# Kernel tuning notes

Measured on AMD Instinct MI355X. Metric: run time of the kernel, lower is better.

Reference implementation:

```python
import jax, jax.numpy as jnp
import numpy as np

NUM_EXPERTS = 4


def _conv1x1(w, b, x):
    # w: [out,in], b: [out], x: [B,in,H,W]
    return jnp.einsum('oc,bchw->bohw', w, x) + b[None, :, None, None]


def _sobel(x):
    c = x.shape[1]
    kx = jnp.array([[-1., 0., 1.], [-2., 0., 2.], [-1., 0., 1.]], dtype=x.dtype)
    ky = jnp.array([[-1., -2., -1.], [0., 0., 0.], [1., 2., 1.]], dtype=x.dtype)
    wx = jnp.broadcast_to(kx[None, None], (c, 1, 3, 3))
    wy = jnp.broadcast_to(ky[None, None], (c, 1, 3, 3))
    dn = ('NCHW', 'OIHW', 'NCHW')
    gx = jax.lax.conv_general_dilated(x, wx, (1, 1), [(1, 1), (1, 1)],
                                      dimension_numbers=dn, feature_group_count=c)
    gy = jax.lax.conv_general_dilated(x, wy, (1, 1), [(1, 1), (1, 1)],
                                      dimension_numbers=dn, feature_group_count=c)
    return gx, gy


def _bilinear_sample(x, gx, gy):
    # torch F.grid_sample(mode='bilinear', padding_mode='zeros', align_corners=False)
    # x: [B,C,H,W]; gx, gy: [B,Hs,Ws] normalized coords in [-1,1]
    B, C, H, W = x.shape
    ix = ((gx + 1.0) * W - 1.0) * 0.5
    iy = ((gy + 1.0) * H - 1.0) * 0.5
    x0 = jnp.floor(ix)
    y0 = jnp.floor(iy)
    wx1 = ix - x0
    wx0 = 1.0 - wx1
    wy1 = iy - y0
    wy0 = 1.0 - wy1
    xf = x.reshape(B, C, H * W)

    def gather(xc, yc):
        valid = (xc >= 0) & (xc <= W - 1) & (yc >= 0) & (yc <= H - 1)
        xi = jnp.clip(xc, 0, W - 1).astype(jnp.int32)
        yi = jnp.clip(yc, 0, H - 1).astype(jnp.int32)
        idx = yi * W + xi  # [B,Hs,Ws]
        v = jax.vmap(lambda xb, ib: xb[:, ib])(xf, idx)  # [B,C,Hs,Ws]
        return v * valid[:, None].astype(x.dtype)

    return (gather(x0, y0) * (wx0 * wy0)[:, None]
            + gather(x0 + 1, y0) * (wx1 * wy0)[:, None]
            + gather(x0, y0 + 1) * (wx0 * wy1)[:, None]
            + gather(x0 + 1, y0 + 1) * (wx1 * wy1)[:, None])


def _forward(x, wc_e, we_e, wb1, bb1, wb2, bb2, wr, br, wo, bo, wcv, bcv, scale, scale2):
    B, c, h, w = x.shape
    sh = round(h * scale)
    sw = round(w * scale2)

    grad_x, grad_y = _sobel(x)

    # relative-offset coordinate embedding, [1,4,sh,sw]
    ih = (jnp.arange(sh, dtype=x.dtype) + 0.5) / scale
    coor_h = ih - jnp.floor(ih + 0.001) - 0.5  # [sh]
    iw = (jnp.arange(sw, dtype=x.dtype) + 0.5) / scale2
    coor_w = iw - jnp.floor(iw + 0.001) - 0.5  # [sw]
    inp = jnp.stack([
        jnp.full((sh, sw), 1.0 / scale2, dtype=x.dtype),
        jnp.full((sh, sw), 1.0 / scale, dtype=x.dtype),
        jnp.broadcast_to(coor_h[:, None], (sh, sw)),
        jnp.broadcast_to(coor_w[None, :], (sh, sw)),
    ], axis=0)[None]

    emb = jax.nn.relu(_conv1x1(wb2, bb2, jax.nn.relu(_conv1x1(wb1, bb1, inp))))
    offset = _conv1x1(wo, bo, emb)                 # [1,2,sh,sw]
    routing = jax.nn.sigmoid(_conv1x1(wr, br, emb))  # [1,E,sh,sw]

    # per-pixel soft mixture of expert compress/expand matrices
    rw = routing.reshape(NUM_EXPERTS, sh * sw).T   # [N,E]
    wc = (rw @ wc_e.reshape(NUM_EXPERTS, -1)).reshape(sh, sw, c // 8, c)
    we = (rw @ we_e.reshape(NUM_EXPERTS, -1)).reshape(sh, sw, c, c // 8)

    feat = _conv1x1(wcv, bcv, jnp.concatenate([x, grad_x, grad_y], axis=1))  # [B,64,h,w]

    # base grid (align_corners=True-style normalization, as in the source) + learned offsets
    gx0 = ((jnp.arange(sw, dtype=x.dtype) + 0.5) / scale2 - 0.5) * 2.0 / (w - 1) - 1.0
    gy0 = ((jnp.arange(sh, dtype=x.dtype) + 0.5) / scale - 0.5) * 2.0 / (h - 1) - 1.0
    gx = jnp.broadcast_to(gx0[None, None, :] + offset[:, 0] * (2.0 / (w - 1)), (B, sh, sw))
    gy = jnp.broadcast_to(gy0[None, :, None] + offset[:, 1] * (2.0 / (h - 1)), (B, sh, sw))

    fea0 = _bilinear_sample(feat, gx, gy)          # [B,64,sh,sw]

    mid = jnp.einsum('hwkc,bchw->bhwk', wc, fea0)  # per-pixel compress (k=C//8)
    out = jnp.einsum('hwck,bhwk->bchw', we, mid)   # per-pixel expand
    return out + fea0


def setup_inputs() -> dict:
    key = jax.random.key(0)
    ks = jax.random.split(key, 13)
    s = 0.05
    return {
        'x': jax.random.normal(ks[0], (2, 64, 192, 192), jnp.float32),
        'weight_compress': jax.random.normal(ks[1], (4, 8, 64), jnp.float32) * s,
        'weight_expand': jax.random.normal(ks[2], (4, 64, 8), jnp.float32) * s,
        'w_body1': jax.random.normal(ks[3], (64, 4), jnp.float32) * s,
        'b_body1': jax.random.normal(ks[4], (64,), jnp.float32) * s,
        'w_body2': jax.random.normal(ks[5], (64, 64), jnp.float32) * s,
        'b_body2': jax.random.normal(ks[6], (64,), jnp.float32) * s,
        'w_routing': jax.random.normal(ks[7], (4, 64), jnp.float32) * s,
        'b_routing': jax.random.normal(ks[8], (4,), jnp.float32) * s,
        'w_offset': jax.random.normal(ks[9], (2, 64), jnp.float32) * s,
        'b_offset': jax.random.normal(ks[10], (2,), jnp.float32) * s,
        'w_conv': jax.random.normal(ks[11], (64, 192), jnp.float32) * s,
        'b_conv': jax.random.normal(ks[12], (64,), jnp.float32) * s,
        'scale': 2,
        'scale2': 2,
    }


def reference(x, weight_compress, weight_expand, w_body1, b_body1, w_body2, b_body2,
              w_routing, b_routing, w_offset, b_offset, w_conv, b_conv, scale, scale2):
    return _forward(x, weight_compress, weight_expand, w_body1, b_body1, w_body2, b_body2,
                    w_routing, b_routing, w_offset, b_offset, w_conv, b_conv, scale, scale2)
```

## Files before the change

### kernel.cpp

```cpp
#include <hip/hip_runtime.h>
#include <hip/hip_bf16.h>
#include <math.h>

#define BN  2
#define CN  64
#define HN  192
#define WN  192
#define SH  384
#define SW  384
#define HW  (HN * WN)
#define NPIX (BN * HN * WN)

typedef __attribute__((ext_vector_type(8))) short bf16x8;
typedef __attribute__((ext_vector_type(4))) float f32x4;

#define CPAD  72
#define TRB   (BN * HN * 3)
#define TBLB  64

__device__ inline unsigned short f2bf(float f) {
    unsigned int u = __float_as_uint(f);
    u += 0x7fffu + ((u >> 16) & 1u);
    return (unsigned short)(u >> 16);
}
__device__ inline unsigned int pkbf(float a, float b) {
    return (unsigned int)f2bf(a) | ((unsigned int)f2bf(b) << 16);
}
__device__ inline float bf2f(unsigned short u) {
    return __uint_as_float((unsigned int)u << 16);
}

__device__ inline void run_mlp(int lane, float in0, float in1, float chv, float cwv,
    const float* __restrict__ wb1, const float* __restrict__ bb1,
    const float* __restrict__ wb2, const float* __restrict__ bb2,
    const float* __restrict__ wr,  const float* __restrict__ wo, float p[6])
{
    float4 w1 = ((const float4*)wb1)[lane];
    float h1 = fmaxf(bb1[lane] + w1.x * in0 + w1.y * in1 + w1.z * chv + w1.w * cwv, 0.f);
    const float4* w2row = (const float4*)(wb2 + lane * 64);
    float acc = bb2[lane];
#pragma unroll
    for (int q = 0; q < 16; ++q) {
        float4 wv = w2row[q];
        acc += wv.x * __shfl(h1, q * 4 + 0)
             + wv.y * __shfl(h1, q * 4 + 1)
             + wv.z * __shfl(h1, q * 4 + 2)
             + wv.w * __shfl(h1, q * 4 + 3);
    }
    float h2 = fmaxf(acc, 0.f);
#pragma unroll
    for (int e = 0; e < 4; ++e) p[e] = wr[e * 64 + lane] * h2;
#pragma unroll
    for (int e = 0; e < 2; ++e) p[4 + e] = wo[e * 64 + lane] * h2;
#pragma unroll
    for (int m = 1; m < 64; m <<= 1) {
#pragma unroll
        for (int e = 0; e < 6; ++e) p[e] += __shfl_xor(p[e], m);
    }
}

__global__ __launch_bounds__(256) void prepass_kernel(
    const float* __restrict__ x,
    const float* __restrict__ wcv,
    const float* __restrict__ wb1, const float* __restrict__ bb1,
    const float* __restrict__ wb2, const float* __restrict__ bb2,
    const float* __restrict__ wr,  const float* __restrict__ br,
    const float* __restrict__ wo,  const float* __restrict__ bo,
    const float* __restrict__ wce, const float* __restrict__ wee,
    const int* __restrict__ scale_p, const int* __restrict__ scale2_p,
    unsigned short* __restrict__ xt,
    unsigned short* __restrict__ tblW,
    float* __restrict__ tblEntry, unsigned short* __restrict__ tblM)
{
    __shared__ __attribute__((aligned(16))) unsigned short sm[64 * CPAD];

    int tid  = threadIdx.x;
    int lane = tid & 63;
    int bi = blockIdx.x;

    if (bi < TRB) {
        int jt = bi % 3;
        int t2 = bi / 3;
        int i  = t2 % HN;
        int b  = t2 / HN;
        int j0 = jt * 64;
        int w  = tid >> 6;
        int c0 = w * 16;

        const float* xp = x + (size_t)b * CN * HW + (size_t)i * WN + j0 + lane;
#pragma unroll
        for (int k = 0; k < 16; k += 2) {
            float f0 = xp[(size_t)(c0 + k) * HW];
            float f1 = xp[(size_t)(c0 + k + 1) * HW];
            *(unsigned int*)(sm + lane * CPAD + c0 + k) = pkbf(f0, f1);
        }
        __syncthreads();
        size_t obase = (((size_t)b * HN + i) * WN + j0) * 64;
#pragma unroll
        for (int it = 0; it < 2; ++it) {
            int task = tid + it * 256;
            int jj = task >> 3, oc = task & 7;
            uint4 v = *(const uint4*)(sm + jj * CPAD + oc * 8);
            *(uint4*)(xt + obase + (size_t)jj * 64 + oc * 8) = v;
        }
        return;
    }

    if (bi == TRB) {
        const float KXc[9] = {-1.f, 0.f, 1.f, -2.f, 0.f, 2.f, -1.f, 0.f, 1.f};
        const float KYc[9] = {-1.f, -2.f, -1.f, 0.f, 0.f, 0.f, 1.f, 2.f, 1.f};
        int wv = tid >> 6;
        int o  = (wv << 4) + (lane & 15);
        const float* wp = wcv + o * 192;
        float v0[2][8], v1[2][8], v2[2][8];
#pragma unroll
        for (int kc = 0; kc < 2; ++kc) {
            int kb = kc * 32 + (lane >> 4) * 8;
            float4 a0 = *(const float4*)(wp + kb);
            float4 a1 = *(const float4*)(wp + kb + 4);
            float4 b0 = *(const float4*)(wp + 64 + kb);
            float4 b1 = *(const float4*)(wp + 64 + kb + 4);
            float4 c0 = *(const float4*)(wp + 128 + kb);
            float4 c1 = *(const float4*)(wp + 128 + kb + 4);
            v0[kc][0]=a0.x; v0[kc][1]=a0.y; v0[kc][2]=a0.z; v0[kc][3]=a0.w;
            v0[kc][4]=a1.x; v0[kc][5]=a1.y; v0[kc][6]=a1.z; v0[kc][7]=a1.w;
            v1[kc][0]=b0.x; v1[kc][1]=b0.y; v1[kc][2]=b0.z; v1[kc][3]=b0.w;
            v1[kc][4]=b1.x; v1[kc][5]=b1.y; v1[kc][6]=b1.z; v1[kc][7]=b1.w;
            v2[kc][0]=c0.x; v2[kc][1]=c0.y; v2[kc][2]=c0.z; v2[kc][3]=c0.w;
            v2[kc][4]=c1.x; v2[kc][5]=c1.y; v2[kc][6]=c1.z; v2[kc][7]=c1.w;
        }
#pragma unroll
        for (int t = 0; t < 9; ++t) {
#pragma unroll
            for (int kc = 0; kc < 2; ++kc) {
                bf16x8 a;
#pragma unroll
                for (int e = 0; e < 8; ++e) {
                    float f = v1[kc][e] * KXc[t] + v2[kc][e] * KYc[t];
                    if (t == 4) f += v0[kc][e];
                    a[e] = (short)f2bf(f);
                }
                *(bf16x8*)(void*)(tblW + (size_t)(((wv * 9 + t) * 2 + kc) * 64 + lane) * 8) = a;
            }
        }
        return;
    }

    {
        float* wcmL = (float*)sm;
        float* wemL = wcmL + 1024;
        float* reL  = wemL + 1024;

        int sc = scale_p[0], sc2 = scale2_p[0];
        float scale = (float)sc, scale2 = (float)sc2;
        float in0 = 1.f / scale2, in1 = 1.f / scale;
        bool fast = (sc2 == 2 && sc <= 16);
        int tb = bi - (TRB + 1);

        if (fast) {
            int pi = tb;
            if (pi >= sc) return;
            if (tid < 64) {
                float ih = (pi + 0.5f) / scale;
                float chv = ih - floorf(ih + 0.001f) - 0.5f;
                float p0[6], p1[6];
                {
                    float iw = 0.5f / scale2;
                    float cwv = iw - floorf(iw + 0.001f) - 0.5f;
                    run_mlp(lane, in0, in1, chv, cwv, wb1, bb1, wb2, bb2, wr, wo, p0);
                }
                {
                    float iw = 1.5f / scale2;
                    float cwv = iw - floorf(iw + 0.001f) - 0.5f;
                    run_mlp(lane, in0, in1, chv, cwv, wb1, bb1, wb2, bb2, wr, wo, p1);
                }
                if (lane == 0) {
                    float* t0 = tblEntry + (pi * 2 + 0) * 8;
                    float* t1 = tblEntry + (pi * 2 + 1) * 8;
#pragma unroll
                    for (int e = 0; e < 4; ++e) {
                        float rE = 1.f / (1.f + expf(-(p0[e] + br[e])));
                        float rO = 1.f / (1.f + expf(-(p1[e] + br[e])));
                        t0[e] = rE; t1[e] = rO;
                        reL[e] = rE; reL[4 + e] = rO;
                    }
                    t0[4] = p0[4] + bo[0]; t0[5] = p0[5] + bo[1];
                    t1[4] = p1[4] + bo[0]; t1[5] = p1[5] + bo[1];
                }
            }
            __syncthreads();
            float reE0 = reL[0], reE1 = reL[1], reE2 = reL[2], reE3 = reL[3];
            float reO0 = reL[4], reO1 = reL[5], reO2 = reL[6], reO3 = reL[7];
            for (int idx = tid; idx < 512; idx += 256) {
                float a = wce[idx], bq = wce[512 + idx], c = wce[1024 + idx], d = wce[1536 + idx];
                wcmL[idx]       = reE0 * a + reE1 * bq + reE2 * c + reE3 * d;
                wcmL[512 + idx] = reO0 * a + reO1 * bq + reO2 * c + reO3 * d;
                float e_ = wee[idx], f = wee[512 + idx], g = wee[1024 + idx], h = wee[1536 + idx];
                wemL[idx]       = reE0 * e_ + reE1 * f + reE2 * g + reE3 * h;
                wemL[512 + idx] = reO0 * e_ + reO1 * f + reO2 * g + reO3 * h;
            }
            __syncthreads();
            int co  = tid >> 2;
            int ci0 = (tid & 3) << 4;
            float w0[8], w1[8];
#pragma unroll
            for (int k = 0; k < 8; ++k) {
                w0[k] = wemL[co * 8 + k];
                w1[k] = wemL[512 + co * 8 + k];
            }
            unsigned short* tbp = tblM + (size_t)pi * 2 * 4096;
#pragma unroll
            for (int cc = 0; cc < 16; ++cc) {
                int ci = ci0 + cc;
                float m0 = 0.f, m1 = 0.f;
#pragma unroll
                for (int k = 0; k < 8; ++k) {
                    m0 += w0[k] * wcmL[k * 64 + ci];
                    m1 += w1[k] * wcmL[512 + k * 64 + ci];
                }
                float avg = 0.5f * (m0 + m1) + ((co == ci) ? 1.f : 0.f);
                tbp[co * 64 + ci]        = f2bf(avg);
                tbp[4096 + co * 64 + ci] = f2bf(0.5f * (m0 - m1));
            }
        } else {
            int w_ = (tb * 256 + tid) >> 6;
            if (w_ >= sc * sc2) return;
            int pi = w_ / sc2, pj = w_ - pi * sc2;
            float ih = (pi + 0.5f) / scale;
            float chv = ih - floorf(ih + 0.001f) - 0.5f;
            float iw = (pj + 0.5f) / scale2;
            float cwv = iw - floorf(iw + 0.001f) - 0.5f;
            float p[6];
            run_mlp(lane, in0, in1, chv, cwv, wb1, bb1, wb2, bb2, wr, wo, p);
            if (lane == 0) {
                float* tp = tblEntry + w_ * 8;
#pragma unroll
                for (int e = 0; e < 4; ++e) tp[e] = 1.f / (1.f + expf(-(p[e] + br[e])));
                tp[4] = p[4] + bo[0];
                tp[5] = p[5] + bo[1];
            }
        }
    }
}

__global__ __launch_bounds__(256) void feat_kernel(
    const unsigned short* __restrict__ xt,
    const unsigned short* __restrict__ tblW,
    const float* __restrict__ bcv,
    unsigned short* __restrict__ featN)
{
    __shared__ __attribute__((aligned(16))) unsigned short sm[198 * CPAD];

    int tid  = threadIdx.x;
    int lane = tid & 63;
    int bi = blockIdx.x;
    int jt = bi % 3;
    int t2 = bi / 3;
    int i0 = t2 % HN;
    int b  = t2 / HN;
    int j0 = jt * 64;
    int w  = __builtin_amdgcn_readfirstlane(tid >> 6);

    int row = lane & 15;
    int q   = lane >> 4;

    bf16x8 afrag[9][2];
#pragma unroll
    for (int t = 0; t < 9; ++t)
#pragma unroll
        for (int kc = 0; kc < 2; ++kc)
            afrag[t][kc] = *(const bf16x8*)(void*)(
                tblW + (size_t)(((w * 9 + t) * 2 + kc) * 64 + lane) * 8);

#pragma unroll
    for (int it = 0; it < 7; ++it) {
        int task = tid + it * 256;
        if (task < 198 * 8) {
            int p  = task >> 3;
            int oc = task & 7;
            int rowi = p / 66;
            int col  = p - rowi * 66;
            int sr = i0 - 1 + rowi;
            int hc = j0 - 1 + col;
            bool ok = (sr >= 0) && (sr < HN) && (hc >= 0) && (hc < WN);
            int srb = ok ? sr : 0;
            int hcb = ok ? hc : 0;
            uint4 v = *(const uint4*)(xt + (((size_t)b * HN + srb) * WN + hcb) * 64 + oc * 8);
            if (!ok) v = (uint4){0u, 0u, 0u, 0u};
            *(uint4*)(sm + p * CPAD + oc * 8) = v;
        }
    }

    __syncthreads();

    f32x4 acc[4] = {};
    const unsigned short* bb0 = sm + row * CPAD + (q << 3);
#pragma unroll
    for (int nt = 0; nt < 4; ++nt) {
#pragma unroll
        for (int t = 0; t < 9; ++t) {
            int a_ = t / 3, dxi = t - a_ * 3;
#pragma unroll
            for (int kc = 0; kc < 2; ++kc) {
                bf16x8 bv = *(const bf16x8*)(bb0 + (a_ * 66 + nt * 16 + dxi) * CPAD + kc * 32);
                acc[nt] = __builtin_amdgcn_mfma_f32_16x16x32_bf16(afrag[t][kc], bv, acc[nt], 0, 0, 0);
            }
        }
    }

    __syncthreads();
    {
        int oc0 = (w << 4) + (q << 2);
        float b0 = bcv[oc0], b1 = bcv[oc0 + 1], b2 = bcv[oc0 + 2], b3 = bcv[oc0 + 3];
#pragma unroll
        for (int nt = 0; nt < 4; ++nt) {
            int px = nt * 16 + row;
            uint2 uu;
            uu.x = pkbf(acc[nt][0] + b0, acc[nt][1] + b1);
            uu.y = pkbf(acc[nt][2] + b2, acc[nt][3] + b3);
            *(uint2*)(sm + px * CPAD + oc0) = uu;
        }
    }
    __syncthreads();
    {
        size_t obase = ((size_t)b * HN + i0) * WN + j0;
#pragma unroll
        for (int it = 0; it < 2; ++it) {
            int task = tid + it * 256;
            int px = task >> 3, oc = task & 7;
            uint4 v = *(const uint4*)(sm + px * CPAD + oc * 8);
            *(uint4*)(featN + (obase + px) * 64 + oc * 8) = v;
        }
    }
}

#define BKP 72
__global__ __launch_bounds__(256) void out_kernel(
    const unsigned short* __restrict__ featN,
    const float* __restrict__ tblEntry,
    const unsigned short* __restrict__ tblM,
    const float* __restrict__ wce,
    const float* __restrict__ wee,
    const int* __restrict__ scale_p, const int* __restrict__ scale2_p,
    float* __restrict__ out)
{
    __shared__ __attribute__((aligned(16))) unsigned short Bsv[64 * BKP];
    __shared__ int   cidx[4 * 64];
    __shared__ float cwt[4 * 64];
    float* midp = (float*)Bsv;

    int Bk = blockIdx.x;
    int T = gridDim.x;
    int t = ((T & 7) == 0) ? ((Bk & 7) * (T >> 3) + (Bk >> 3)) : Bk;

    int tid = threadIdx.x;
    int g = __builtin_amdgcn_readfirstlane(tid >> 6);
    int lane = tid & 63;
    int pix0 = t * 64;
    int b = pix0 / (SH * SW);
    int r0 = pix0 - b * SH * SW;
    int i = r0 / SW;
    int j0 = r0 - i * SW;

    int sc = scale_p[0], sc2 = scale2_p[0];
    float scale = (float)sc, scale2 = (float)sc2;
    int pi = i - (i / sc) * sc;
    const float inv_wm1 = 2.f / (float)(WN - 1);
    const float inv_hm1 = 2.f / (float)(HN - 1);

    bool fast = (sc2 == 2 && sc <= 16);
    if (fast) {
        if (tid < 64) {
            int px = tid;
            int jpx = j0 + px;
            int pjx = jpx - (jpx / sc2) * sc2;
            int entry = pi * sc2 + pjx;
            float offx = tblEntry[entry * 8 + 4];
            float offy = tblEntry[entry * 8 + 5];
            float gx = ((jpx + 0.5f) / scale2 - 0.5f) * inv_wm1 - 1.f + offx * inv_wm1;
            float gy = ((i + 0.5f) / scale  - 0.5f) * inv_hm1 - 1.f + offy * inv_hm1;
            float ix = ((gx + 1.f) * WN - 1.f) * 0.5f;
            float iy = ((gy + 1.f) * HN - 1.f) * 0.5f;
            float fx0 = floorf(ix), fy0 = floorf(iy);
            int x0 = (int)fx0, y0 = (int)fy0;
            float wx1 = ix - fx0, wx0 = 1.f - wx1;
            float wy1 = iy - fy0, wy0 = 1.f - wy1;
            bool vx0 = (x0 >= 0) && (x0 <= WN - 1);
            bool vx1 = (x0 + 1 >= 0) && (x0 + 1 <= WN - 1);
            bool vy0 = (y0 >= 0) && (y0 <= HN - 1);
            bool vy1 = (y0 + 1 >= 0) && (y0 + 1 <= HN - 1);
            int x0c = min(max(x0, 0), WN - 1);
            int x1c = min(max(x0 + 1, 0), WN - 1);
            int y0c = min(max(y0, 0), HN - 1);
            int y1c = min(max(y0 + 1, 0), HN - 1);
            cidx[0 * 64 + px] = y0c * WN + x0c;
            cidx[1 * 64 + px] = y0c * WN + x1c;
            cidx[2 * 64 + px] = y1c * WN + x0c;
            cidx[3 * 64 + px] = y1c * WN + x1c;
            cwt[0 * 64 + px] = wx0 * wy0 * ((vx0 && vy0) ? 1.f : 0.f);
            cwt[1 * 64 + px] = wx1 * wy0 * ((vx1 && vy0) ? 1.f : 0.f);
            cwt[2 * 64 + px] = wx0 * wy1 * ((vx0 && vy1) ? 1.f : 0.f);
            cwt[3 * 64 + px] = wx1 * wy1 * ((vx1 && vy1) ? 1.f : 0.f);
        }

        int row = lane & 15;
        int kb  = (lane >> 4) << 3;
        const unsigned short* Mb = tblM + (size_t)pi * 2 * 4096 + (g * 16 + row) * 64 + kb;
        bf16x8 a1[2], a2[2];
        a1[0] = *(const bf16x8*)(Mb);
        a1[1] = *(const bf16x8*)(Mb + 32);
        a2[0] = *(const bf16x8*)(Mb + 4096);
        a2[1] = *(const bf16x8*)(Mb + 4096 + 32);

        __syncthreads();

        const unsigned short* fb = featN + (size_t)b * HW * 64;
#pragma unroll
        for (int it = 0; it < 2; ++it) {
            int task = tid + it * 256;
            int px = task >> 3, oct = task & 7;
            const unsigned short* fo = fb + oct * 8;
            float a8[8] = {};
#pragma unroll
            for (int k = 0; k < 4; ++k) {
                bf16x8 cv = *(const bf16x8*)(fo + (size_t)cidx[k * 64 + px] * 64);
                float wk = cwt[k * 64 + px];
#pragma unroll
                for (int e = 0; e < 8; ++e)
                    a8[e] += wk * bf2f((unsigned short)cv[e]);
            }
            uint4 pk;
            pk.x = pkbf(a8[0], a8[1]);
            pk.y = pkbf(a8[2], a8[3]);
            pk.z = pkbf(a8[4], a8[5]);
            pk.w = pkbf(a8[6], a8[7]);
            *(uint4*)(Bsv + px * BKP + oct * 8) = pk;
        }

        __syncthreads();

        f32x4 acc1[4] = {}, acc2[4] = {};
        const unsigned short* bp = Bsv + (lane & 15) * BKP + kb;
#pragma unroll
        for (int nt = 0; nt < 4; ++nt) {
            const unsigned short* bnt = bp + nt * 16 * BKP;
#pragma unroll
            for (int ks = 0; ks < 2; ++ks) {
                bf16x8 bf = *(const bf16x8*)(bnt + ks * 32);
                acc1[nt] = __builtin_amdgcn_mfma_f32_16x16x32_bf16(a1[ks], bf, acc1[nt], 0, 0, 0);
                acc2[nt] = __builtin_amdgcn_mfma_f32_16x16x32_bf16(a2[ks], bf, acc2[nt], 0, 0, 0);
            }
        }

        int q = lane >> 4;
#pragma unroll
        for (int rr = 0; rr < 4; ++rr) {
            int c = g * 16 + q * 4 + rr;
            size_t rowb = (size_t)(b * CN + c) * SH * SW + r0;
#pragma unroll
            for (int nt = 0; nt < 4; ++nt) {
                int n = (lane & 15) + nt * 16;
                float sgn = (n & 1) ? -1.f : 1.f;
                out[rowb + n] = acc1[nt][rr] + sgn * acc2[nt][rr];
            }
        }
    } else {
        int j = j0 + lane;
        int r = r0 + lane;
        int pj = j - (j / sc2) * sc2;
        int entry = pi * sc2 + pj;
        float offx = tblEntry[entry * 8 + 4];
        float offy = tblEntry[entry * 8 + 5];
        float gx = ((j + 0.5f) / scale2 - 0.5f) * inv_wm1 - 1.f + offx * inv_wm1;
        float gy = ((i + 0.5f) / scale  - 0.5f) * inv_hm1 - 1.f + offy * inv_hm1;
        float ix = ((gx + 1.f) * WN - 1.f) * 0.5f;
        float iy = ((gy + 1.f) * HN - 1.f) * 0.5f;
        float fx0 = floorf(ix), fy0 = floorf(iy);
        int x0 = (int)fx0, y0 = (int)fy0;
        float wx1 = ix - fx0, wx0 = 1.f - wx1;
        float wy1 = iy - fy0, wy0 = 1.f - wy1;
        bool vx0 = (x0 >= 0) && (x0 <= WN - 1);
        bool vx1 = (x0 + 1 >= 0) && (x0 + 1 <= WN - 1);
        bool vy0 = (y0 >= 0) && (y0 <= HN - 1);
        bool vy1 = (y0 + 1 >= 0) && (y0 + 1 <= HN - 1);
        int x0c = min(max(x0, 0), WN - 1);
        int x1c = min(max(x0 + 1, 0), WN - 1);
        int y0c = min(max(y0, 0), HN - 1);
        int y1c = min(max(y0 + 1, 0), HN - 1);
        float w00 = wx0 * wy0 * ((vx0 && vy0) ? 1.f : 0.f);
        float w10 = wx1 * wy0 * ((vx1 && vy0) ? 1.f : 0.f);
        float w01 = wx0 * wy1 * ((vx0 && vy1) ? 1.f : 0.f);
        float w11 = wx1 * wy1 * ((vx1 && vy1) ? 1.f : 0.f);
        const unsigned short* fb = featN + ((size_t)b * HW) * 64;
        const unsigned short* p00 = fb + (size_t)(y0c * WN + x0c) * 64;
        const unsigned short* p10 = fb + (size_t)(y0c * WN + x1c) * 64;
        const unsigned short* p01 = fb + (size_t)(y1c * WN + x0c) * 64;
        const unsigned short* p11 = fb + (size_t)(y1c * WN + x1c) * 64;

        float f0[16];
#pragma unroll
        for (int cc = 0; cc < 16; ++cc) {
            int c = g * 16 + cc;
            f0[cc] = bf2f(p00[c]) * w00 + bf2f(p10[c]) * w10
                   + bf2f(p01[c]) * w01 + bf2f(p11[c]) * w11;
        }

        float4 rw = *(const float4*)(tblEntry + entry * 8);
        float re[4] = {rw.x, rw.y, rw.z, rw.w};
        float part[4][8];
#pragma unroll
        for (int e = 0; e < 4; ++e) {
#pragma unroll
            for (int k = 0; k < 8; ++k) {
                const float* wrow = wce + (e * 8 + k) * 64 + g * 16;
                float d = 0.f;
#pragma unroll
                for (int cc = 0; cc < 16; ++cc) d += wrow[cc] * f0[cc];
                part[e][k] = d;
            }
        }
#pragma unroll
        for (int k = 0; k < 8; ++k) {
            float m = re[0] * part[0][k] + re[1] * part[1][k]
                    + re[2] * part[2][k] + re[3] * part[3][k];
            midp[(g * 64 + lane) * 9 + k] = m;
        }
        __syncthreads();
        float mid[8];
#pragma unroll
        for (int k = 0; k < 8; ++k)
            mid[k] = midp[(0 * 64 + lane) * 9 + k] + midp[(1 * 64 + lane) * 9 + k]
                   + midp[(2 * 64 + lane) * 9 + k] + midp[(3 * 64 + lane) * 9 + k];
#pragma unroll
        for (int cc = 0; cc < 16; ++cc) {
            int c = g * 16 + cc;
            float v = f0[cc];
#pragma unroll
            for (int e = 0; e < 4; ++e) {
                const float* wrow = wee + (e * 64 + c) * 8;
                float d = 0.f;
#pragma unroll
                for (int k = 0; k < 8; ++k) d += wrow[k] * mid[k];
                v += re[e] * d;
            }
            out[(size_t)(b * CN + c) * SH * SW + r] = v;
        }
    }
}

extern "C" void kernel_launch(void* const* d_in, const int* in_sizes, int n_in,
                              void* d_out, int out_size, void* d_ws, size_t ws_size,
                              hipStream_t stream) {
    const float* x    = (const float*)d_in[0];
    const float* wce  = (const float*)d_in[1];
    const float* wee  = (const float*)d_in[2];
    const float* wb1  = (const float*)d_in[3];
    const float* bb1  = (const float*)d_in[4];
    const float* wb2  = (const float*)d_in[5];
    const float* bb2  = (const float*)d_in[6];
    const float* wr   = (const float*)d_in[7];
    const float* br   = (const float*)d_in[8];
    const float* wo   = (const float*)d_in[9];
    const float* bo   = (const float*)d_in[10];
    const float* wcv  = (const float*)d_in[11];
    const float* bcv  = (const float*)d_in[12];
    const int*   scale  = (const int*)d_in[13];
    const int*   scale2 = (const int*)d_in[14];
    float* out = (float*)d_out;

    unsigned short* featN = (unsigned short*)d_ws;
    float* tblEntry = (float*)((char*)d_ws + (size_t)BN * HW * 64 * 2);
    unsigned short* tblM = (unsigned short*)((char*)tblEntry + 2048 * 4);
    unsigned short* tblW = tblM + 16 * 2 * 4096;
    unsigned short* xt   = tblW + 4 * 9 * 2 * 64 * 8;

    prepass_kernel<<<TRB + 1 + TBLB, 256, 0, stream>>>(
        x, wcv, wb1, bb1, wb2, bb2, wr, br, wo, bo,
        wce, wee, scale, scale2, xt, tblW, tblEntry, tblM);
    feat_kernel<<<TRB, 256, 0, stream>>>(xt, tblW, bcv, featN);
    out_kernel<<<BN * SH * SW / 64, 256, 0, stream>>>(featN, tblEntry, tblM,
                                                      wce, wee, scale, scale2, out);
}
```

Before: 152.0 us.

## Fuse NCHW-to-NHWC bf16 transpose into feat kernel halo load

Removes the transpose blocks from the prepass kernel, so the x-to-bf16 channels-last intermediate buffer is no longer written and re-read. The feat kernel now reads fp32 NCHW input directly for its 3x66 halo tile and converts it to bf16 in shared memory. This drops a global round trip of the transposed tensor and shrinks the prepass launch. In exchange, only 198 of 256 threads load, each doing 64 strided channel reads, and each input row is re-read by three neighbouring row blocks in fp32.

```diff
diff --git a/kernel.cpp b/kernel.cpp
--- a/kernel.cpp
+++ b/kernel.cpp
@@ -60,7 +60,6 @@
 }
 
 __global__ __launch_bounds__(256) void prepass_kernel(
-    const float* __restrict__ x,
     const float* __restrict__ wcv,
     const float* __restrict__ wb1, const float* __restrict__ bb1,
     const float* __restrict__ wb2, const float* __restrict__ bb2,
@@ -68,45 +67,16 @@
     const float* __restrict__ wo,  const float* __restrict__ bo,
     const float* __restrict__ wce, const float* __restrict__ wee,
     const int* __restrict__ scale_p, const int* __restrict__ scale2_p,
-    unsigned short* __restrict__ xt,
     unsigned short* __restrict__ tblW,
     float* __restrict__ tblEntry, unsigned short* __restrict__ tblM)
 {
-    __shared__ __attribute__((aligned(16))) unsigned short sm[64 * CPAD];
+    __shared__ __attribute__((aligned(16))) float smf[2056];
 
     int tid  = threadIdx.x;
     int lane = tid & 63;
     int bi = blockIdx.x;
 
-    if (bi < TRB) {
-        int jt = bi % 3;
-        int t2 = bi / 3;
-        int i  = t2 % HN;
-        int b  = t2 / HN;
-        int j0 = jt * 64;
-        int w  = tid >> 6;
-        int c0 = w * 16;
-
-        const float* xp = x + (size_t)b * CN * HW + (size_t)i * WN + j0 + lane;
-#pragma unroll
-        for (int k = 0; k < 16; k += 2) {
-            float f0 = xp[(size_t)(c0 + k) * HW];
-            float f1 = xp[(size_t)(c0 + k + 1) * HW];
-            *(unsigned int*)(sm + lane * CPAD + c0 + k) = pkbf(f0, f1);
-        }
-        __syncthreads();
-        size_t obase = (((size_t)b * HN + i) * WN + j0) * 64;
-#pragma unroll
-        for (int it = 0; it < 2; ++it) {
-            int task = tid + it * 256;
-            int jj = task >> 3, oc = task & 7;
-            uint4 v = *(const uint4*)(sm + jj * CPAD + oc * 8);
-            *(uint4*)(xt + obase + (size_t)jj * 64 + oc * 8) = v;
-        }
-        return;
-    }
-
-    if (bi == TRB) {
+    if (bi == 0) {
         const float KXc[9] = {-1.f, 0.f, 1.f, -2.f, 0.f, 2.f, -1.f, 0.f, 1.f};
         const float KYc[9] = {-1.f, -2.f, -1.f, 0.f, 0.f, 0.f, 1.f, 2.f, 1.f};
         int wv = tid >> 6;
@@ -147,7 +117,7 @@
     }
 
     {
-        float* wcmL = (float*)sm;
+        float* wcmL = smf;
         float* wemL = wcmL + 1024;
         float* reL  = wemL + 1024;
 
@@ -155,7 +125,7 @@
         float scale = (float)sc, scale2 = (float)sc2;
         float in0 = 1.f / scale2, in1 = 1.f / scale;
         bool fast = (sc2 == 2 && sc <= 16);
-        int tb = bi - (TRB + 1);
+        int tb = bi - 1;
 
         if (fast) {
             int pi = tb;
@@ -244,7 +214,7 @@
 }
 
 __global__ __launch_bounds__(256) void feat_kernel(
-    const unsigned short* __restrict__ xt,
+    const float* __restrict__ x,
     const unsigned short* __restrict__ tblW,
     const float* __restrict__ bcv,
     unsigned short* __restrict__ featN)
@@ -272,22 +242,35 @@
             afrag[t][kc] = *(const bf16x8*)(void*)(
                 tblW + (size_t)(((w * 9 + t) * 2 + kc) * 64 + lane) * 8);
 
-#pragma unroll
-    for (int it = 0; it < 7; ++it) {
-        int task = tid + it * 256;
-        if (task < 198 * 8) {
-            int p  = task >> 3;
-            int oc = task & 7;
-            int rowi = p / 66;
-            int col  = p - rowi * 66;
-            int sr = i0 - 1 + rowi;
-            int hc = j0 - 1 + col;
-            bool ok = (sr >= 0) && (sr < HN) && (hc >= 0) && (hc < WN);
-            int srb = ok ? sr : 0;
-            int hcb = ok ? hc : 0;
-            uint4 v = *(const uint4*)(xt + (((size_t)b * HN + srb) * WN + hcb) * 64 + oc * 8);
-            if (!ok) v = (uint4){0u, 0u, 0u, 0u};
-            *(uint4*)(sm + p * CPAD + oc * 8) = v;
+    if (tid < 3 * 66) {
+        int rowi = tid / 66;
+        int col  = tid - rowi * 66;
+        int sr = i0 - 1 + rowi;
+        bool rok = (sr >= 0) && (sr < HN);
+        int src = rok ? sr : 0;
+        int hc = j0 - 1 + col;
+        bool cok = (hc >= 0) && (hc < WN);
+        int hcc = cok ? hc : 0;
+        float msk = (rok && cok) ? 1.f : 0.f;
+        const float* p = x + (size_t)b * CN * HW + (size_t)src * WN + hcc;
+        unsigned short* xrow = sm + tid * CPAD;
+#pragma unroll 4
+        for (int k = 0; k < 8; ++k) {
+            float a0 = p[0]              * msk;
+            float a1 = p[(size_t)HW]     * msk;
+            float a2 = p[2 * (size_t)HW] * msk;
+            float a3 = p[3 * (size_t)HW] * msk;
+            float a4 = p[4 * (size_t)HW] * msk;
+            float a5 = p[5 * (size_t)HW] * msk;
+            float a6 = p[6 * (size_t)HW] * msk;
+            float a7 = p[7 * (size_t)HW] * msk;
+            uint4 uu;
+            uu.x = pkbf(a0, a1);
+            uu.y = pkbf(a2, a3);
+            uu.z = pkbf(a4, a5);
+            uu.w = pkbf(a6, a7);
+            *(uint4*)(xrow + (k << 3)) = uu;
+            p += 8 * (size_t)HW;
         }
     }
 
@@ -572,12 +555,11 @@
     float* tblEntry = (float*)((char*)d_ws + (size_t)BN * HW * 64 * 2);
     unsigned short* tblM = (unsigned short*)((char*)tblEntry + 2048 * 4);
     unsigned short* tblW = tblM + 16 * 2 * 4096;
-    unsigned short* xt   = tblW + 4 * 9 * 2 * 64 * 8;
-
-    prepass_kernel<<<TRB + 1 + TBLB, 256, 0, stream>>>(
-        x, wcv, wb1, bb1, wb2, bb2, wr, br, wo, bo,
-        wce, wee, scale, scale2, xt, tblW, tblEntry, tblM);
-    feat_kernel<<<TRB, 256, 0, stream>>>(xt, tblW, bcv, featN);
+
+    prepass_kernel<<<1 + TBLB, 256, 0, stream>>>(
+        wcv, wb1, bb1, wb2, bb2, wr, br, wo, bo,
+        wce, wee, scale, scale2, tblW, tblEntry, tblM);
+    feat_kernel<<<TRB, 256, 0, stream>>>(x, tblW, bcv, featN);
     out_kernel<<<BN * SH * SW / 64, 256, 0, stream>>>(featN, tblEntry, tblM,
                                                       wce, wee, scale, scale2, out);
 }
```

Result: no change. 152.4 us (+0.3%).
